# Performance work log

Measured on AMD Instinct MI355X. Metric: run time of the kernel, lower is better.

Reference implementation:

```python
import jax, jax.numpy as jnp
import numpy as np

KS = [3, 3, 7, 7, 11, 11, 21, 21]  # TEXT_KERNEL_SIZES
KMAX = 21
H = 8
D_MODEL = 1024
D_H = D_MODEL // H
R = 4
B = 2
N = 4096


def _extract_windows_1d(xh, k):
    # xh: (B, n, d_h) -> windows: (B, n, k, d_h), zero-padded, stride 1
    pad = k // 2
    xp = jnp.pad(xh, ((0, 0), (pad, pad), (0, 0)))
    idx = jnp.arange(xh.shape[1])[:, None] + jnp.arange(k)[None, :]  # (n, k)
    return xp[:, idx]  # (B, n, k, d_h)


def setup_inputs() -> dict:
    key = jax.random.key(0)
    ks = jax.random.split(key, 10)
    s = 0.02
    return {
        "x": jax.random.normal(ks[0], (B, N, D_MODEL), dtype=jnp.float32),
        "W_in": jax.random.normal(ks[1], (D_MODEL, D_MODEL), dtype=jnp.float32) * s,
        "b_in": jnp.zeros((D_MODEL,), dtype=jnp.float32),
        "W_out": jax.random.normal(ks[2], (D_MODEL, D_MODEL), dtype=jnp.float32) * (0.02 / np.sqrt(2.0 * 8)),
        "b_out": jnp.zeros((D_MODEL,), dtype=jnp.float32),
        "Wc": jax.random.normal(ks[3], (H, D_H, R), dtype=jnp.float32) * s,  # per-token coeff proj
        "A": jax.random.normal(ks[4], (H, R, KMAX), dtype=jnp.float32) * s,  # rank -> kernel-pos factor (padded to KMAX)
        "V": jax.random.normal(ks[5], (H, R, D_H), dtype=jnp.float32) * s,   # rank -> channel factor
        "base": jax.random.normal(ks[6], (H, KMAX, D_H), dtype=jnp.float32) * s,  # static kernel (padded)
        "alphas": jnp.zeros((H,), dtype=jnp.float32),  # sigmoid gate params
    }


def reference(x, W_in, b_in, W_out, b_out, Wc, A, V, base, alphas):
    Bsz, n, d = x.shape
    x_proj = x @ W_in.T + b_in                        # (B, n, d_model)
    x_heads = x_proj.reshape(Bsz, n, H, D_H)          # (B, n, H, d_h)
    head_outs = []
    for h in range(H):
        k = KS[h]
        x_h = x_heads[:, :, h, :]                     # (B, n, d_h)
        # Factored per-token kernel generation
        c = x_h @ Wc[h]                               # (B, n, R)
        dyn = jnp.einsum('bnr,rk,rd->bnkd', c, A[h, :, :k], V[h])  # (B, n, k, d_h)
        alpha = jax.nn.sigmoid(alphas[h])
        K_hat = alpha * dyn + (1.0 - alpha) * base[h, :k][None, None]  # (B, n, k, d_h)
        windows = _extract_windows_1d(x_h, k)         # (B, n, k, d_h)
        o_h = jnp.einsum('bnkd,bnkd->bnd', K_hat, windows)
        head_outs.append(o_h)
    concat = jnp.concatenate(head_outs, axis=-1)      # (B, n, d_model)
    return concat @ W_out.T + b_out
```

## Files before the change

kernel.cpp:

```cpp
#include <hip/hip_runtime.h>
#include <stdint.h>

typedef __bf16 bf16;
typedef __bf16 bf16x8 __attribute__((ext_vector_type(8)));
typedef float f32x4 __attribute__((ext_vector_type(4)));

#define AS1 __attribute__((address_space(1)))
#define AS3 __attribute__((address_space(3)))

__device__ __forceinline__ void gload_lds16(const void* g, void* l) {
    __builtin_amdgcn_global_load_lds((const AS1 uint32_t*)g, (AS3 uint32_t*)l, 16, 0, 0);
}

#define BM 128
#define BN 128
#define BK 64

template <typename OT>
__global__ __launch_bounds__(256, 2) void gemm_nt(
    const bf16* __restrict__ A, const bf16* __restrict__ B,
    const float* __restrict__ bias, OT* __restrict__ C,
    int M, int N, int K)
{
    __shared__ bf16 smA[BM * BK];
    __shared__ bf16 smB[BN * BK];

    const int tid  = threadIdx.x;
    const int wave = tid >> 6;
    const int lane = tid & 63;
    const int wm = (wave >> 1) * 64;
    const int wn = (wave & 1) * 64;
    const int rowA0 = blockIdx.x * BM;
    const int rowB0 = blockIdx.y * BN;

    f32x4 acc[4][4] = {};

    const int g  = lane >> 4;
    const int rm = lane & 15;

    for (int k0 = 0; k0 < K; k0 += BK) {
        #pragma unroll
        for (int i = 0; i < 4; ++i) {
            int slot = i * 256 + tid;
            int row  = slot >> 3;
            int kgs  = slot & 7;
            int kd   = kgs ^ ((row >> 1) & 7);
            const bf16* ga = A + (size_t)(rowA0 + row) * K + k0 + kd * 8;
            const bf16* gb = B + (size_t)(rowB0 + row) * K + k0 + kd * 8;
            int ldsbase = (i * 256 + (wave << 6)) * 8;
            gload_lds16(ga, &smA[ldsbase]);
            gload_lds16(gb, &smB[ldsbase]);
        }
        __syncthreads();

        #pragma unroll
        for (int s = 0; s < 2; ++s) {
            bf16x8 af[4], bfr[4];
            #pragma unroll
            for (int mi = 0; mi < 4; ++mi) {
                int row  = wm + mi * 16 + rm;
                int slot = row * 8 + ((s * 4 + g) ^ ((row >> 1) & 7));
                af[mi] = *(const bf16x8*)&smA[slot * 8];
            }
            #pragma unroll
            for (int ni = 0; ni < 4; ++ni) {
                int row  = wn + ni * 16 + rm;
                int slot = row * 8 + ((s * 4 + g) ^ ((row >> 1) & 7));
                bfr[ni] = *(const bf16x8*)&smB[slot * 8];
            }
            #pragma unroll
            for (int mi = 0; mi < 4; ++mi)
                #pragma unroll
                for (int ni = 0; ni < 4; ++ni)
                    acc[mi][ni] = __builtin_amdgcn_mfma_f32_16x16x32_bf16(
                        af[mi], bfr[ni], acc[mi][ni], 0, 0, 0);
        }
        __syncthreads();
    }

    const int quad = lane >> 4;
    #pragma unroll
    for (int ni = 0; ni < 4; ++ni) {
        int col = rowB0 + wn + ni * 16 + rm;
        float bcol = bias[col];
        #pragma unroll
        for (int mi = 0; mi < 4; ++mi) {
            #pragma unroll
            for (int r = 0; r < 4; ++r) {
                int rowc = rowA0 + wm + mi * 16 + quad * 4 + r;
                C[(size_t)rowc * N + col] = (OT)(acc[mi][ni][r] + bcol);
            }
        }
    }
}

__global__ void cast_all_kernel(const float* __restrict__ x, bf16* __restrict__ xb,
                                const float* __restrict__ wi, bf16* __restrict__ wib,
                                const float* __restrict__ wo, bf16* __restrict__ wob)
{
    const int NX8 = (2 * 4096 * 1024) / 8;
    const int NW8 = (1024 * 1024) / 8;
    int i = blockIdx.x * 256 + threadIdx.x;
    const float* in; bf16* out; int idx;
    if (i < NX8)            { in = x;  out = xb;  idx = i; }
    else if (i < NX8 + NW8) { in = wi; out = wib; idx = i - NX8; }
    else                    { in = wo; out = wob; idx = i - NX8 - NW8; }
    const float4* p = (const float4*)in;
    float4 a = p[2 * idx], b = p[2 * idx + 1];
    bf16x8 o;
    o[0] = (bf16)a.x; o[1] = (bf16)a.y; o[2] = (bf16)a.z; o[3] = (bf16)a.w;
    o[4] = (bf16)b.x; o[5] = (bf16)b.y; o[6] = (bf16)b.z; o[7] = (bf16)b.w;
    *(bf16x8*)(out + 8 * idx) = o;
}

__global__ __launch_bounds__(256) void c_compute(
    const bf16* __restrict__ xpb, const float* __restrict__ Wc,
    float* __restrict__ cbuf)
{
    const int wave = threadIdx.x >> 6, lane = threadIdx.x & 63;
    const int row  = blockIdx.x * 4 + wave;
    const int h    = lane >> 3;
    const int d0   = (lane & 7) * 16;

    const bf16* xr = xpb + (size_t)row * 1024 + lane * 16;
    bf16x8 v0 = *(const bf16x8*)xr;
    bf16x8 v1 = *(const bf16x8*)(xr + 8);
    float p0 = 0.f, p1 = 0.f, p2 = 0.f, p3 = 0.f;
    #pragma unroll
    for (int i = 0; i < 16; ++i) {
        float xv = (i < 8) ? (float)v0[i & 7] : (float)v1[i & 7];
        float4 wr = *(const float4*)(Wc + h * 512 + (d0 + i) * 4);
        p0 += xv * wr.x; p1 += xv * wr.y; p2 += xv * wr.z; p3 += xv * wr.w;
    }
    #pragma unroll
    for (int off = 1; off <= 4; off <<= 1) {
        p0 += __shfl_xor(p0, off);
        p1 += __shfl_xor(p1, off);
        p2 += __shfl_xor(p2, off);
        p3 += __shfl_xor(p3, off);
    }
    if ((lane & 7) == 0) {
        float4 o = {p0, p1, p2, p3};
        *(float4*)(cbuf + (size_t)row * 32 + h * 4) = o;
    }
}

__constant__ int KS_c[8] = {3, 3, 7, 7, 11, 11, 21, 21};

template <int K>
__device__ __forceinline__ void mix_body(
    int h, int d, int n0, const bf16* __restrict__ xpb,
    const float* __restrict__ cbuf, const float* __restrict__ Aw,
    const float* __restrict__ Vw, const float* __restrict__ basew,
    float alpha, bf16* __restrict__ y)
{
    constexpr int T = 8;
    constexpr int W = T + K - 1;
    constexpr int pad = K / 2;
    const int nloc = n0 & 4095;

    float w[W];
    #pragma unroll
    for (int j = 0; j < W; ++j) {
        int nl = nloc + j - pad;
        bool valid = (nl >= 0) && (nl < 4096);
        w[j] = valid ? (float)xpb[(size_t)(n0 + j - pad) * 1024 + h * 128 + d] : 0.f;
    }

    float s0[T] = {}, s1[T] = {}, s2[T] = {}, s3[T] = {}, tv[T] = {};
    const float* Ah = Aw + h * 84;
    const float* bh = basew + h * 2688 + d;
    #pragma unroll
    for (int j = 0; j < K; ++j) {
        float a0 = Ah[j], a1 = Ah[21 + j], a2 = Ah[42 + j], a3 = Ah[63 + j];
        float bbj = bh[j * 128];
        #pragma unroll
        for (int t = 0; t < T; ++t) {
            float x = w[t + j];
            s0[t] += a0 * x; s1[t] += a1 * x;
            s2[t] += a2 * x; s3[t] += a3 * x;
            tv[t] += bbj * x;
        }
    }

    float v0 = Vw[h * 512 + d],       v1 = Vw[h * 512 + 128 + d];
    float v2 = Vw[h * 512 + 256 + d], v3 = Vw[h * 512 + 384 + d];
    #pragma unroll
    for (int t = 0; t < T; ++t) {
        float4 c4 = *(const float4*)(cbuf + (size_t)(n0 + t) * 32 + h * 4);
        float o = alpha * (c4.x * v0 * s0[t] + c4.y * v1 * s1[t] +
                           c4.z * v2 * s2[t] + c4.w * v3 * s3[t])
                + (1.f - alpha) * tv[t];
        y[(size_t)(n0 + t) * 1024 + h * 128 + d] = (bf16)o;
    }
}

__global__ __launch_bounds__(256) void head_mix2(
    const bf16* __restrict__ xpb, const float* __restrict__ cbuf,
    const float* __restrict__ Aw, const float* __restrict__ Vw,
    const float* __restrict__ basew, const float* __restrict__ alphas,
    bf16* __restrict__ y)
{
    const int h   = blockIdx.x;
    const int d   = threadIdx.x & 127;
    const int sub = threadIdx.x >> 7;
    const int n0  = (blockIdx.y * 2 + sub) * 8;
    const float alpha = 1.f / (1.f + __expf(-alphas[h]));

    switch (KS_c[h]) {
        case 3:  mix_body<3>(h, d, n0, xpb, cbuf, Aw, Vw, basew, alpha, y); break;
        case 7:  mix_body<7 >(h, d, n0, xpb, cbuf, Aw, Vw, basew, alpha, y); break;
        case 11: mix_body<11>(h, d, n0, xpb, cbuf, Aw, Vw, basew, alpha, y); break;
        default: mix_body<21>(h, d, n0, xpb, cbuf, Aw, Vw, basew, alpha, y); break;
    }
}

extern "C" void kernel_launch(void* const* d_in, const int* in_sizes, int n_in,
                              void* d_out, int out_size, void* d_ws, size_t ws_size,
                              hipStream_t stream)
{
    const float* x      = (const float*)d_in[0];
    const float* W_in   = (const float*)d_in[1];
    const float* b_in   = (const float*)d_in[2];
    const float* W_out  = (const float*)d_in[3];
    const float* b_out  = (const float*)d_in[4];
    const float* Wc     = (const float*)d_in[5];
    const float* Aw     = (const float*)d_in[6];
    const float* Vw     = (const float*)d_in[7];
    const float* basew  = (const float*)d_in[8];
    const float* alphas = (const float*)d_in[9];
    float* out = (float*)d_out;

    const size_t MB = 1u << 20;
    char* ws = (char*)d_ws;
    bf16*  xb   = (bf16*) (ws);
    bf16*  wib  = (bf16*) (ws + 16 * MB);
    bf16*  wob  = (bf16*) (ws + 18 * MB);
    bf16*  xpb  = (bf16*) (ws + 20 * MB);
    bf16*  yb   = (bf16*) (ws + 36 * MB);
    float* cbuf = (float*)(ws + 52 * MB);

    const int NTOT8 = (2 * 4096 * 1024 + 2 * 1024 * 1024) / 8;

    cast_all_kernel<<<NTOT8 / 256, 256, 0, stream>>>(x, xb, W_in, wib, W_out, wob);

    gemm_nt<bf16><<<dim3(8192 / BM, 1024 / BN), 256, 0, stream>>>(
        xb, wib, b_in, xpb, 8192, 1024, 1024);

    c_compute<<<8192 / 4, 256, 0, stream>>>(xpb, Wc, cbuf);

    head_mix2<<<dim3(8, 512), 256, 0, stream>>>(
        xpb, cbuf, Aw, Vw, basew, alphas, yb);

    gemm_nt<float><<<dim3(8192 / BM, 1024 / BN), 256, 0, stream>>>(
        yb, wob, b_out, out, 8192, 1024, 1024);
}
```

Before: 207.3 us.

## Shrink GEMM N-tile to 64 and stage head-mix windows through LDS

The GEMM tile narrows from 128x128 to 128x64 with an occupancy hint of 4 blocks per CU, which doubles the number of blocks and halves per-wave accumulators. The head-mix kernel now loads each block's 16-row window plus halo into LDS with async global-to-LDS copies, then reads the sliding-window inputs from shared memory instead of issuing strided global loads per thread. The grid is transposed so row blocks vary fastest. Smaller GEMM tiles lower data reuse per block, and the LDS staging adds a barrier.

```diff
diff --git a/kernel.cpp b/kernel.cpp
--- a/kernel.cpp
+++ b/kernel.cpp
@@ -13,11 +13,11 @@
 }
 
 #define BM 128
-#define BN 128
+#define BN 64
 #define BK 64
 
 template <typename OT>
-__global__ __launch_bounds__(256, 2) void gemm_nt(
+__global__ __launch_bounds__(256, 4) void gemm_nt(
     const bf16* __restrict__ A, const bf16* __restrict__ B,
     const float* __restrict__ bias, OT* __restrict__ C,
     int M, int N, int K)
@@ -29,11 +29,11 @@
     const int wave = tid >> 6;
     const int lane = tid & 63;
     const int wm = (wave >> 1) * 64;
-    const int wn = (wave & 1) * 64;
+    const int wn = (wave & 1) * 32;
     const int rowA0 = blockIdx.x * BM;
     const int rowB0 = blockIdx.y * BN;
 
-    f32x4 acc[4][4] = {};
+    f32x4 acc[4][2] = {};
 
     const int g  = lane >> 4;
     const int rm = lane & 15;
@@ -43,19 +43,23 @@
         for (int i = 0; i < 4; ++i) {
             int slot = i * 256 + tid;
             int row  = slot >> 3;
-            int kgs  = slot & 7;
-            int kd   = kgs ^ ((row >> 1) & 7);
-            const bf16* ga = A + (size_t)(rowA0 + row) * K + k0 + kd * 8;
-            const bf16* gb = B + (size_t)(rowB0 + row) * K + k0 + kd * 8;
-            int ldsbase = (i * 256 + (wave << 6)) * 8;
-            gload_lds16(ga, &smA[ldsbase]);
-            gload_lds16(gb, &smB[ldsbase]);
+            int kg   = slot & 7;
+            int kd   = kg ^ ((row >> 1) & 7);
+            gload_lds16(A + (size_t)(rowA0 + row) * K + k0 + kd * 8, &smA[slot * 8]);
+        }
+        #pragma unroll
+        for (int i = 0; i < 2; ++i) {
+            int slot = i * 256 + tid;
+            int row  = slot >> 3;
+            int kg   = slot & 7;
+            int kd   = kg ^ ((row >> 1) & 7);
+            gload_lds16(B + (size_t)(rowB0 + row) * K + k0 + kd * 8, &smB[slot * 8]);
         }
         __syncthreads();
 
         #pragma unroll
         for (int s = 0; s < 2; ++s) {
-            bf16x8 af[4], bfr[4];
+            bf16x8 af[4], bfr[2];
             #pragma unroll
             for (int mi = 0; mi < 4; ++mi) {
                 int row  = wm + mi * 16 + rm;
@@ -63,7 +67,7 @@
                 af[mi] = *(const bf16x8*)&smA[slot * 8];
             }
             #pragma unroll
-            for (int ni = 0; ni < 4; ++ni) {
+            for (int ni = 0; ni < 2; ++ni) {
                 int row  = wn + ni * 16 + rm;
                 int slot = row * 8 + ((s * 4 + g) ^ ((row >> 1) & 7));
                 bfr[ni] = *(const bf16x8*)&smB[slot * 8];
@@ -71,7 +75,7 @@
             #pragma unroll
             for (int mi = 0; mi < 4; ++mi)
                 #pragma unroll
-                for (int ni = 0; ni < 4; ++ni)
+                for (int ni = 0; ni < 2; ++ni)
                     acc[mi][ni] = __builtin_amdgcn_mfma_f32_16x16x32_bf16(
                         af[mi], bfr[ni], acc[mi][ni], 0, 0, 0);
         }
@@ -80,7 +84,7 @@
 
     const int quad = lane >> 4;
     #pragma unroll
-    for (int ni = 0; ni < 4; ++ni) {
+    for (int ni = 0; ni < 2; ++ni) {
         int col = rowB0 + wn + ni * 16 + rm;
         float bcol = bias[col];
         #pragma unroll
@@ -148,23 +152,43 @@
 __constant__ int KS_c[8] = {3, 3, 7, 7, 11, 11, 21, 21};
 
 template <int K>
-__device__ __forceinline__ void mix_body(
-    int h, int d, int n0, const bf16* __restrict__ xpb,
+__device__ __forceinline__ void mix_body3(
+    int h, int tid, int r0, const bf16* __restrict__ xpb,
     const float* __restrict__ cbuf, const float* __restrict__ Aw,
     const float* __restrict__ Vw, const float* __restrict__ basew,
-    float alpha, bf16* __restrict__ y)
-{
-    constexpr int T = 8;
-    constexpr int W = T + K - 1;
+    float alpha, bf16* __restrict__ y, bf16* sx)
+{
+    constexpr int T   = 8;
     constexpr int pad = K / 2;
-    const int nloc = n0 & 4095;
-
-    float w[W];
-    #pragma unroll
-    for (int j = 0; j < W; ++j) {
-        int nl = nloc + j - pad;
-        bool valid = (nl >= 0) && (nl < 4096);
-        w[j] = valid ? (float)xpb[(size_t)(n0 + j - pad) * 1024 + h * 128 + d] : 0.f;
+    constexpr int R   = 16 + 2 * pad;
+    constexpr int S   = R * 16;
+    constexpr int NP  = (S + 255) / 256;
+
+    #pragma unroll
+    for (int p = 0; p < NP; ++p) {
+        int slot = p * 256 + tid;
+        if (slot < S) {
+            int lrow = slot >> 4;
+            int lc   = slot & 15;
+            int grow = r0 - pad + lrow;
+            grow = min(max(grow, 0), 8191);
+            gload_lds16(xpb + (size_t)grow * 1024 + h * 128 + lc * 8,
+                        sx + slot * 8);
+        }
+    }
+    __syncthreads();
+
+    const int d   = tid & 127;
+    const int sub = tid >> 7;
+    const int lr0 = sub * 8;
+    const int nb  = (r0 & 4095) + sub * 8;
+
+    float w[T + K - 1];
+    #pragma unroll
+    for (int j = 0; j < T + K - 1; ++j) {
+        int nl = nb + j - pad;
+        float v = (float)sx[(lr0 + j) * 128 + d];
+        w[j] = (nl >= 0 && nl < 4096) ? v : 0.f;
     }
 
     float s0[T] = {}, s1[T] = {}, s2[T] = {}, s3[T] = {}, tv[T] = {};
@@ -187,31 +211,31 @@
     float v2 = Vw[h * 512 + 256 + d], v3 = Vw[h * 512 + 384 + d];
     #pragma unroll
     for (int t = 0; t < T; ++t) {
-        float4 c4 = *(const float4*)(cbuf + (size_t)(n0 + t) * 32 + h * 4);
+        int rowo = r0 + sub * 8 + t;
+        float4 c4 = *(const float4*)(cbuf + (size_t)rowo * 32 + h * 4);
         float o = alpha * (c4.x * v0 * s0[t] + c4.y * v1 * s1[t] +
                            c4.z * v2 * s2[t] + c4.w * v3 * s3[t])
                 + (1.f - alpha) * tv[t];
-        y[(size_t)(n0 + t) * 1024 + h * 128 + d] = (bf16)o;
-    }
-}
-
-__global__ __launch_bounds__(256) void head_mix2(
+        y[(size_t)rowo * 1024 + h * 128 + d] = (bf16)o;
+    }
+}
+
+__global__ __launch_bounds__(256, 4) void head_mix3(
     const bf16* __restrict__ xpb, const float* __restrict__ cbuf,
     const float* __restrict__ Aw, const float* __restrict__ Vw,
     const float* __restrict__ basew, const float* __restrict__ alphas,
     bf16* __restrict__ y)
 {
-    const int h   = blockIdx.x;
-    const int d   = threadIdx.x & 127;
-    const int sub = threadIdx.x >> 7;
-    const int n0  = (blockIdx.y * 2 + sub) * 8;
+    __shared__ bf16 sx[36 * 128];
+    const int h  = blockIdx.y;
+    const int r0 = blockIdx.x * 16;
     const float alpha = 1.f / (1.f + __expf(-alphas[h]));
 
     switch (KS_c[h]) {
-        case 3:  mix_body<3>(h, d, n0, xpb, cbuf, Aw, Vw, basew, alpha, y); break;
-        case 7:  mix_body<7 >(h, d, n0, xpb, cbuf, Aw, Vw, basew, alpha, y); break;
-        case 11: mix_body<11>(h, d, n0, xpb, cbuf, Aw, Vw, basew, alpha, y); break;
-        default: mix_body<21>(h, d, n0, xpb, cbuf, Aw, Vw, basew, alpha, y); break;
+        case 3:  mix_body3<3 >(h, threadIdx.x, r0, xpb, cbuf, Aw, Vw, basew, alpha, y, sx); break;
+        case 7:  mix_body3<7 >(h, threadIdx.x, r0, xpb, cbuf, Aw, Vw, basew, alpha, y, sx); break;
+        case 11: mix_body3<11>(h, threadIdx.x, r0, xpb, cbuf, Aw, Vw, basew, alpha, y, sx); break;
+        default: mix_body3<21>(h, threadIdx.x, r0, xpb, cbuf, Aw, Vw, basew, alpha, y, sx); break;
     }
 }
 
@@ -249,7 +273,7 @@
 
     c_compute<<<8192 / 4, 256, 0, stream>>>(xpb, Wc, cbuf);
 
-    head_mix2<<<dim3(8, 512), 256, 0, stream>>>(
+    head_mix3<<<dim3(512, 8), 256, 0, stream>>>(
         xpb, cbuf, Aw, Vw, basew, alphas, yb);
 
     gemm_nt<float><<<dim3(8192 / BM, 1024 / BN), 256, 0, stream>>>(
```

After: 178.4 us. 1.16x faster.
